# Kernel tuning notes

Measured on AMD Instinct MI355X. Metric: run time of the kernel, lower is better.

## Reference

```python
import jax, jax.numpy as jnp
import numpy as np

B = 16384
IN = 1024      # 2*input_dim
H = 1024       # hidden_dim
K = IN + H     # gate input size


def setup_inputs() -> dict:
    key = jax.random.key(0)
    ks = jax.random.split(key, 20)
    x = jax.random.normal(ks[0], (B, IN), dtype=jnp.float32)
    n_id = jax.random.randint(ks[1], (B,), 0, 16384, dtype=jnp.int64) if jax.config.jax_enable_x64 else jax.random.randint(ks[1], (B,), 0, 16384).astype(jnp.int32)
    t = jax.random.uniform(ks[2], (B,), dtype=jnp.float32)
    last_t = jnp.zeros((B,), dtype=jnp.float32)
    s = 1.0 / np.sqrt(K)
    def lin(k):
        k1, k2 = jax.random.split(k)
        W = jax.random.uniform(k1, (K, H), minval=-s, maxval=s, dtype=jnp.float32)
        b = jax.random.uniform(k2, (H,), minval=-s, maxval=s, dtype=jnp.float32)
        return W, b
    Wi, bi = lin(ks[3])
    Wit, bit = lin(ks[4])
    Wf, bf = lin(ks[5])
    Wft, bft = lin(ks[6])
    Wz, bz = lin(ks[7])
    Wo, bo = lin(ks[8])
    Wd, bd = lin(ks[9])
    return dict(x=x, n_id=n_id, t=t, last_t=last_t,
                Wi=Wi, bi=bi, Wit=Wit, bit=bit, Wf=Wf, bf=bf,
                Wft=Wft, bft=bft, Wz=Wz, bz=bz, Wo=Wo, bo=bo, Wd=Wd, bd=bd)


def reference(x, n_id, t, last_t, Wi, bi, Wit, bit, Wf, bf, Wft, bft, Wz, bz, Wo, bo, Wd, bd):
    batch = x.shape[0]
    h = jnp.zeros((batch, H), dtype=x.dtype)
    c = jnp.zeros((batch, H), dtype=x.dtype)
    c_target = jnp.zeros((batch, H), dtype=x.dtype)

    k = jnp.concatenate([x, h], axis=1)  # [B, K]
    # fuse 7 gate GEMMs into one: [B,K] @ [K,7H]
    W = jnp.concatenate([Wi, Wit, Wf, Wft, Wz, Wo, Wd], axis=1)
    b = jnp.concatenate([bi, bit, bf, bft, bz, bo, bd])
    g = k @ W + b  # [B, 7H]
    gi, git, gf, gft, gz, go, gd = jnp.split(g, 7, axis=1)

    gate_i = jax.nn.sigmoid(gi)
    gate_i_target = jax.nn.sigmoid(git)
    gate_f = jax.nn.sigmoid(gf)
    gate_f_target = jax.nn.sigmoid(gft)
    gate_o = jax.nn.sigmoid(go)
    z = 2.0 * jax.nn.sigmoid(gz) - 1.0
    c_n = gate_f * c + gate_i * z
    c_target_n = gate_f_target * c_target + gate_i_target * z
    delta = jax.nn.softplus(gd)

    delta_t = (t - last_t)[:, None]  # [B,1]
    cell = c_target_n + (c_n - c_target_n) * jnp.exp(-delta * delta_t)
    h_n = gate_o * jnp.tanh(cell)
    return (h_n, c_n, c_target_n, gate_o, delta)
```

## Files before the change

kernel.cpp:

```cpp
#include <hip/hip_runtime.h>


#define B_SZ 16384
#define H_SZ 1024
#define K_SZ 1024
#define BH ((size_t)B_SZ * H_SZ)
#define NGATE 5

typedef __bf16 bf16x8 __attribute__((ext_vector_type(8)));
typedef float f32x4 __attribute__((ext_vector_type(4)));

__device__ __forceinline__ unsigned short f2bf(float f) {
    unsigned int u = __float_as_uint(f);
    u += 0x7FFFu + ((u >> 16) & 1u);
    return (unsigned short)(u >> 16);
}

__device__ __forceinline__ float sigm(float x) {
    return 1.f / (1.f + __expf(-x));
}
__device__ __forceinline__ float softplus_f(float x) {
    return fmaxf(x, 0.f) + __logf(1.f + __expf(-fabsf(x)));
}
__device__ __forceinline__ float tanh_f(float x) {
    float e = __expf(2.f * x);
    return (e - 1.f) / (e + 1.f);
}

__global__ void conv_x_kernel(const float* __restrict__ x, unsigned short* __restrict__ xb) {
    int i = blockIdx.x * blockDim.x + threadIdx.x;
    float4 v = ((const float4*)x)[i];
    ushort4 o;
    o.x = f2bf(v.x); o.y = f2bf(v.y); o.z = f2bf(v.z); o.w = f2bf(v.w);
    ((ushort4*)xb)[i] = o;
}

__global__ void conv_w_kernel(const float* __restrict__ W0, const float* __restrict__ W1,
                              const float* __restrict__ W2, const float* __restrict__ W3,
                              const float* __restrict__ W4, unsigned short* __restrict__ wt) {
    const float* Ws[NGATE] = {W0, W1, W2, W3, W4};
    const float* W = Ws[blockIdx.z];
    __shared__ float tile[32][33];
    const int k0 = blockIdx.x * 32, n0 = blockIdx.y * 32;
    const int r = threadIdx.x >> 5, c = threadIdx.x & 31;
#pragma unroll
    for (int rr = 0; rr < 4; rr++) {
        tile[r + rr * 8][c] = W[(size_t)(k0 + r + rr * 8) * H_SZ + n0 + c];
    }
    __syncthreads();
    unsigned short* out = wt + (size_t)blockIdx.z * H_SZ * K_SZ;
#pragma unroll
    for (int rr = 0; rr < 4; rr++) {
        out[(size_t)(n0 + r + rr * 8) * K_SZ + k0 + c] = f2bf(tile[c][r + rr * 8]);
    }
}

__global__ __launch_bounds__(256, 2) void fused_clstm_kernel(
    const unsigned short* __restrict__ xb,
    const unsigned short* __restrict__ wt,
    const float* __restrict__ bi, const float* __restrict__ bit_,
    const float* __restrict__ bz, const float* __restrict__ bo,
    const float* __restrict__ bd,
    const float* __restrict__ t, const float* __restrict__ last_t,
    float* __restrict__ out)
{
    __shared__ unsigned short smem[(1 + NGATE) * 2048];

    const int tid  = threadIdx.x;
    const int wave = tid >> 6;
    const int lane = tid & 63;
    const int quad = lane >> 4;
    const int l16  = lane & 15;
    const int wm   = wave >> 1;
    const int wn   = wave & 1;
    const int m0   = blockIdx.y * 64;
    const int n0   = blockIdx.x * 64;

    f32x4 acc[NGATE][2][2];
#pragma unroll
    for (int g = 0; g < NGATE; g++)
#pragma unroll
        for (int mf = 0; mf < 2; mf++)
#pragma unroll
            for (int nf = 0; nf < 2; nf++)
                acc[g][mf][nf] = (f32x4){0.f, 0.f, 0.f, 0.f};

    const int srow = lane >> 2;
    const int scol = (lane & 3) * 8;

    for (int k0 = 0; k0 < K_SZ; k0 += 32) {
        __syncthreads();
#pragma unroll
        for (int i = 0; i < 6; i++) {
            const int c = wave * 6 + i;
            const unsigned short* gsrc;
            if (c < 4) {
                gsrc = xb + (size_t)(m0 + c * 16 + srow) * K_SZ + k0 + scol;
            } else {
                const int g = (c - 4) >> 2, q = (c - 4) & 3;
                gsrc = wt + (size_t)g * H_SZ * K_SZ
                          + (size_t)(n0 + q * 16 + srow) * K_SZ + k0 + scol;
            }
            __builtin_amdgcn_global_load_lds(
                (const __attribute__((address_space(1))) unsigned int*)gsrc,
                (__attribute__((address_space(3))) unsigned int*)(&smem[c * 512 + lane * 8]),
                16, 0, 0);
        }
        __syncthreads();

        bf16x8 a0 = *(const bf16x8*)(&smem[(wm * 32      + l16) * 32 + quad * 8]);
        bf16x8 a1 = *(const bf16x8*)(&smem[(wm * 32 + 16 + l16) * 32 + quad * 8]);
#pragma unroll
        for (int g = 0; g < NGATE; g++) {
            const unsigned short* bs = &smem[(1 + g) * 2048];
            bf16x8 b0 = *(const bf16x8*)(&bs[(wn * 32      + l16) * 32 + quad * 8]);
            bf16x8 b1 = *(const bf16x8*)(&bs[(wn * 32 + 16 + l16) * 32 + quad * 8]);
            acc[g][0][0] = __builtin_amdgcn_mfma_f32_16x16x32_bf16(a0, b0, acc[g][0][0], 0, 0, 0);
            acc[g][1][0] = __builtin_amdgcn_mfma_f32_16x16x32_bf16(a1, b0, acc[g][1][0], 0, 0, 0);
            acc[g][0][1] = __builtin_amdgcn_mfma_f32_16x16x32_bf16(a0, b1, acc[g][0][1], 0, 0, 0);
            acc[g][1][1] = __builtin_amdgcn_mfma_f32_16x16x32_bf16(a1, b1, acc[g][1][1], 0, 0, 0);
        }
    }

    const float* biasp[NGATE] = {bi, bit_, bz, bo, bd};
    float bv[NGATE][2];
#pragma unroll
    for (int g = 0; g < NGATE; g++)
#pragma unroll
        for (int nf = 0; nf < 2; nf++)
            bv[g][nf] = biasp[g][n0 + wn * 32 + nf * 16 + l16];

#pragma unroll
    for (int mf = 0; mf < 2; mf++) {
#pragma unroll
        for (int r = 0; r < 4; r++) {
            const int brow = m0 + wm * 32 + mf * 16 + quad * 4 + r;
            const float dt = t[brow] - last_t[brow];
#pragma unroll
            for (int nf = 0; nf < 2; nf++) {
                const int ncol = n0 + wn * 32 + nf * 16 + l16;
                const float gi  = acc[0][mf][nf][r] + bv[0][nf];
                const float git = acc[1][mf][nf][r] + bv[1][nf];
                const float gz  = acc[2][mf][nf][r] + bv[2][nf];
                const float go  = acc[3][mf][nf][r] + bv[3][nf];
                const float gd  = acc[4][mf][nf][r] + bv[4][nf];

                const float gate_i  = sigm(gi);
                const float gate_it = sigm(git);
                const float z       = 2.f * sigm(gz) - 1.f;
                const float gate_o  = sigm(go);
                const float delta   = softplus_f(gd);

                const float c_n  = gate_i  * z;
                const float ct_n = gate_it * z;
                const float cell = ct_n + (c_n - ct_n) * __expf(-delta * dt);
                const float h_n  = gate_o * tanh_f(cell);

                const size_t idx = (size_t)brow * H_SZ + ncol;
                out[idx]          = h_n;
                out[BH + idx]     = c_n;
                out[2 * BH + idx] = ct_n;
                out[3 * BH + idx] = gate_o;
                out[4 * BH + idx] = delta;
            }
        }
    }
}

extern "C" void kernel_launch(void* const* d_in, const int* in_sizes, int n_in,
                              void* d_out, int out_size, void* d_ws, size_t ws_size,
                              hipStream_t stream) {
    const float* x      = (const float*)d_in[0];
    const float* t      = (const float*)d_in[2];
    const float* last_t = (const float*)d_in[3];
    const float* Wi  = (const float*)d_in[4];
    const float* bi  = (const float*)d_in[5];
    const float* Wit = (const float*)d_in[6];
    const float* bit_= (const float*)d_in[7];
    const float* Wz  = (const float*)d_in[12];
    const float* bz  = (const float*)d_in[13];
    const float* Wo  = (const float*)d_in[14];
    const float* bo  = (const float*)d_in[15];
    const float* Wd  = (const float*)d_in[16];
    const float* bd  = (const float*)d_in[17];

    unsigned short* xb = (unsigned short*)d_ws;
    unsigned short* wt = xb + (size_t)B_SZ * K_SZ;

    conv_x_kernel<<<(B_SZ * K_SZ / 4) / 256, 256, 0, stream>>>(x, xb);

    dim3 gw(32, 32, NGATE);
    conv_w_kernel<<<gw, 256, 0, stream>>>(Wi, Wit, Wz, Wo, Wd, wt);

    dim3 gm(H_SZ / 64, B_SZ / 64);
    fused_clstm_kernel<<<gm, 256, 0, stream>>>(xb, wt, bi, bit_, bz, bo, bd,
                                               t, last_t, (float*)d_out);
}
```

Before: 653.2 us.

## Enlarge GEMM block tile to 128 rows, vectorize weight transpose, use fast reciprocal

The fused gate GEMM block tile grows from 64 to 128 batch rows, so each wave computes 4x2 MFMA fragments per gate and each staged weight tile is reused across twice as many rows. This cuts global weight traffic and raises MFMA work per LDS load. The cost is double the accumulator registers (160 floats), which may lower occupancy or cause spills under launch_bounds(256,2). The weight conversion kernel now uses 64x64 tiles with ushort4 stores, and the sigmoid and tanh divisions become hardware reciprocal approximations.

```diff
diff --git a/kernel.cpp b/kernel.cpp
--- a/kernel.cpp
+++ b/kernel.cpp
@@ -16,15 +16,14 @@
     return (unsigned short)(u >> 16);
 }
 
-__device__ __forceinline__ float sigm(float x) {
-    return 1.f / (1.f + __expf(-x));
-}
+__device__ __forceinline__ float rcp_fast(float x) { return __builtin_amdgcn_rcpf(x); }
+__device__ __forceinline__ float sigm(float x) { return rcp_fast(1.f + __expf(-x)); }
 __device__ __forceinline__ float softplus_f(float x) {
     return fmaxf(x, 0.f) + __logf(1.f + __expf(-fabsf(x)));
 }
 __device__ __forceinline__ float tanh_f(float x) {
     float e = __expf(2.f * x);
-    return (e - 1.f) / (e + 1.f);
+    return (e - 1.f) * rcp_fast(e + 1.f);
 }
 
 __global__ void conv_x_kernel(const float* __restrict__ x, unsigned short* __restrict__ xb) {
@@ -40,18 +39,31 @@
                               const float* __restrict__ W4, unsigned short* __restrict__ wt) {
     const float* Ws[NGATE] = {W0, W1, W2, W3, W4};
     const float* W = Ws[blockIdx.z];
-    __shared__ float tile[32][33];
-    const int k0 = blockIdx.x * 32, n0 = blockIdx.y * 32;
-    const int r = threadIdx.x >> 5, c = threadIdx.x & 31;
-#pragma unroll
-    for (int rr = 0; rr < 4; rr++) {
-        tile[r + rr * 8][c] = W[(size_t)(k0 + r + rr * 8) * H_SZ + n0 + c];
+    __shared__ float tile[64][65];
+    const int k0 = blockIdx.x * 64, n0 = blockIdx.y * 64;
+    const int tid = threadIdx.x;
+    {
+        const int kk = tid >> 6, nn = tid & 63;
+#pragma unroll
+        for (int rr = 0; rr < 16; rr++) {
+            const int row = kk * 16 + rr;
+            tile[row][nn] = W[(size_t)(k0 + row) * H_SZ + n0 + nn];
+        }
     }
     __syncthreads();
     unsigned short* out = wt + (size_t)blockIdx.z * H_SZ * K_SZ;
-#pragma unroll
-    for (int rr = 0; rr < 4; rr++) {
-        out[(size_t)(n0 + r + rr * 8) * K_SZ + k0 + c] = f2bf(tile[c][r + rr * 8]);
+    {
+        const int nrow = tid >> 2, kq = (tid & 3) * 16;
+#pragma unroll
+        for (int j = 0; j < 4; j++) {
+            const int k = kq + j * 4;
+            ushort4 v;
+            v.x = f2bf(tile[k + 0][nrow]);
+            v.y = f2bf(tile[k + 1][nrow]);
+            v.z = f2bf(tile[k + 2][nrow]);
+            v.w = f2bf(tile[k + 3][nrow]);
+            *(ushort4*)&out[(size_t)(n0 + nrow) * K_SZ + k0 + k] = v;
+        }
     }
 }
 
@@ -64,7 +76,7 @@
     const float* __restrict__ t, const float* __restrict__ last_t,
     float* __restrict__ out)
 {
-    __shared__ unsigned short smem[(1 + NGATE) * 2048];
+    __shared__ unsigned short smem[28 * 512];
 
     const int tid  = threadIdx.x;
     const int wave = tid >> 6;
@@ -73,14 +85,14 @@
     const int l16  = lane & 15;
     const int wm   = wave >> 1;
     const int wn   = wave & 1;
-    const int m0   = blockIdx.y * 64;
+    const int m0   = blockIdx.y * 128;
     const int n0   = blockIdx.x * 64;
 
-    f32x4 acc[NGATE][2][2];
+    f32x4 acc[NGATE][4][2];
 #pragma unroll
     for (int g = 0; g < NGATE; g++)
 #pragma unroll
-        for (int mf = 0; mf < 2; mf++)
+        for (int mf = 0; mf < 4; mf++)
 #pragma unroll
             for (int nf = 0; nf < 2; nf++)
                 acc[g][mf][nf] = (f32x4){0.f, 0.f, 0.f, 0.f};
@@ -91,13 +103,13 @@
     for (int k0 = 0; k0 < K_SZ; k0 += 32) {
         __syncthreads();
 #pragma unroll
-        for (int i = 0; i < 6; i++) {
-            const int c = wave * 6 + i;
+        for (int i = 0; i < 7; i++) {
+            const int c = wave * 7 + i;
             const unsigned short* gsrc;
-            if (c < 4) {
+            if (c < 8) {
                 gsrc = xb + (size_t)(m0 + c * 16 + srow) * K_SZ + k0 + scol;
             } else {
-                const int g = (c - 4) >> 2, q = (c - 4) & 3;
+                const int g = (c - 8) >> 2, q = (c - 8) & 3;
                 gsrc = wt + (size_t)g * H_SZ * K_SZ
                           + (size_t)(n0 + q * 16 + srow) * K_SZ + k0 + scol;
             }
@@ -108,17 +120,20 @@
         }
         __syncthreads();
 
-        bf16x8 a0 = *(const bf16x8*)(&smem[(wm * 32      + l16) * 32 + quad * 8]);
-        bf16x8 a1 = *(const bf16x8*)(&smem[(wm * 32 + 16 + l16) * 32 + quad * 8]);
+        bf16x8 a[4];
+#pragma unroll
+        for (int mf = 0; mf < 4; mf++)
+            a[mf] = *(const bf16x8*)(&smem[(wm * 64 + mf * 16 + l16) * 32 + quad * 8]);
 #pragma unroll
         for (int g = 0; g < NGATE; g++) {
-            const unsigned short* bs = &smem[(1 + g) * 2048];
+            const unsigned short* bs = &smem[(8 + g * 4) * 512];
             bf16x8 b0 = *(const bf16x8*)(&bs[(wn * 32      + l16) * 32 + quad * 8]);
             bf16x8 b1 = *(const bf16x8*)(&bs[(wn * 32 + 16 + l16) * 32 + quad * 8]);
-            acc[g][0][0] = __builtin_amdgcn_mfma_f32_16x16x32_bf16(a0, b0, acc[g][0][0], 0, 0, 0);
-            acc[g][1][0] = __builtin_amdgcn_mfma_f32_16x16x32_bf16(a1, b0, acc[g][1][0], 0, 0, 0);
-            acc[g][0][1] = __builtin_amdgcn_mfma_f32_16x16x32_bf16(a0, b1, acc[g][0][1], 0, 0, 0);
-            acc[g][1][1] = __builtin_amdgcn_mfma_f32_16x16x32_bf16(a1, b1, acc[g][1][1], 0, 0, 0);
+#pragma unroll
+            for (int mf = 0; mf < 4; mf++) {
+                acc[g][mf][0] = __builtin_amdgcn_mfma_f32_16x16x32_bf16(a[mf], b0, acc[g][mf][0], 0, 0, 0);
+                acc[g][mf][1] = __builtin_amdgcn_mfma_f32_16x16x32_bf16(a[mf], b1, acc[g][mf][1], 0, 0, 0);
+            }
         }
     }
 
@@ -131,10 +146,10 @@
             bv[g][nf] = biasp[g][n0 + wn * 32 + nf * 16 + l16];
 
 #pragma unroll
-    for (int mf = 0; mf < 2; mf++) {
+    for (int mf = 0; mf < 4; mf++) {
 #pragma unroll
         for (int r = 0; r < 4; r++) {
-            const int brow = m0 + wm * 32 + mf * 16 + quad * 4 + r;
+            const int brow = m0 + wm * 64 + mf * 16 + quad * 4 + r;
             const float dt = t[brow] - last_t[brow];
 #pragma unroll
             for (int nf = 0; nf < 2; nf++) {
@@ -189,10 +204,10 @@
 
     conv_x_kernel<<<(B_SZ * K_SZ / 4) / 256, 256, 0, stream>>>(x, xb);
 
-    dim3 gw(32, 32, NGATE);
+    dim3 gw(16, 16, NGATE);
     conv_w_kernel<<<gw, 256, 0, stream>>>(Wi, Wit, Wz, Wo, Wd, wt);
 
-    dim3 gm(H_SZ / 64, B_SZ / 64);
+    dim3 gm(H_SZ / 64, B_SZ / 128);
     fused_clstm_kernel<<<gm, 256, 0, stream>>>(xb, wt, bi, bit_, bz, bo, bd,
                                                t, last_t, (float*)d_out);
 }
```

Result: faster. 609.0 us (-6.8%).
